# Optimization experiments

Measured on AMD Instinct MI355X. Metric: run time of the kernel, lower is better.

## Reference

```python
import jax, jax.numpy as jnp
import numpy as np

H = W = 64
C = 256
NUM_HEADS = 8

# Static index maps from AbsolutePositionalWeighting.__init__
_center_h = (H - 1) // 2
_center_w = (W - 1) // 2
_gi, _gj = np.meshgrid(np.arange(H), np.arange(W), indexing='ij')
_dx = _gi - _center_h
_dy = _gj - _center_w
DH = max(int(np.abs(_dx).max()), _center_h)
DW = max(int(np.abs(_dy).max()), _center_w)
DX_IDX = jnp.asarray(_dx + DH)  # (H, W)
DY_IDX = jnp.asarray(_dy + DW)  # (H, W)


def setup_inputs() -> dict:
    key = jax.random.key(0)
    ks = jax.random.split(key, 6)
    B, N = 16, H * W
    x1 = jax.random.normal(ks[0], (B, N, C), dtype=jnp.float32)
    x2 = jax.random.normal(ks[1], (B, N, C), dtype=jnp.float32)
    x3 = jax.random.normal(ks[2], (B, N, C), dtype=jnp.float32)
    pos_weights = 0.1 * jax.random.normal(ks[3], (2 * DH + 1, 2 * DW + 1, C), dtype=jnp.float32)
    lepe_w = 0.1 * jax.random.normal(ks[4], (C, 1, 3, 3), dtype=jnp.float32)  # depthwise OIHW
    lepe_b = 0.01 * jax.random.normal(ks[5], (C,), dtype=jnp.float32)
    return {"x1": x1, "x2": x2, "x3": x3, "pos_weights": pos_weights,
            "lepe_w": lepe_w, "lepe_b": lepe_b}


def reference(x1, x2, x3, pos_weights, lepe_w, lepe_b):
    b, n, c = x1.shape
    nh, hd = NUM_HEADS, c // NUM_HEADS

    q = jax.nn.elu(x1) + 1.0
    k = jax.nn.elu(x2) + 1.0
    v = x3

    # Positional gating: sigmoid(pos_weights gathered at per-pixel offsets) -> (N, C)
    pw = jax.nn.sigmoid(pos_weights[DX_IDX, DY_IDX, :]).reshape(n, c)
    q_rope = q * pw[None]  # (b, n, c)
    k_rope = k * pw[None]

    # Split heads: (b, n, nh, hd)
    q4 = q.reshape(b, n, nh, hd)
    k4 = k.reshape(b, n, nh, hd)
    v4 = v.reshape(b, n, nh, hd)
    qr4 = q_rope.reshape(b, n, nh, hd)
    kr4 = k_rope.reshape(b, n, nh, hd)

    # Normalizer z = 1 / (q . mean_n(k) + eps)
    k_mean = k4.mean(axis=1)  # (b, nh, hd)
    z = 1.0 / (jnp.einsum('bnhd,bhd->bnh', q4, k_mean) + 1e-6)

    # Linear attention: kv = (k_rope/sqrt(n))^T (v/sqrt(n)); out = q_rope @ kv * z
    kv = jnp.einsum('bnhd,bnhe->bhde', kr4, v4) / n  # (b, nh, hd, hd)
    attn = jnp.einsum('bnhd,bhde->bnhe', qr4, kv) * z[..., None]
    attn = attn.reshape(b, n, c)

    # LePE: depthwise 3x3 conv on v image (NCHW)
    v_img = v.reshape(b, H, W, c).transpose(0, 3, 1, 2)
    lepe = jax.lax.conv_general_dilated(
        v_img, lepe_w, window_strides=(1, 1), padding='SAME',
        feature_group_count=c,
        dimension_numbers=('NCHW', 'OIHW', 'NCHW'))
    lepe = lepe + lepe_b[None, :, None, None]
    lepe = lepe.transpose(0, 2, 3, 1).reshape(b, n, c)

    return attn + lepe
```

## Files before the change

kernel.cpp:

```cpp
#include <hip/hip_runtime.h>

#define BB 16
#define HIMG 64
#define WIMG 64
#define CC 256
#define NHEAD 8
#define HD 32
#define NN 4096
#define PWD 65
#define PADC 264
#define NCH 32

typedef short bf16x8 __attribute__((ext_vector_type(8)));
typedef float f32x4 __attribute__((ext_vector_type(4)));

__device__ __forceinline__ float elu1(float x) {
    return x > 0.0f ? x + 1.0f : __expf(x);
}
__device__ __forceinline__ float sigm(float x) {
    return 1.0f / (1.0f + __expf(-x));
}
__device__ __forceinline__ unsigned short f2bf(float f) {
    union { float f; unsigned int u; } v; v.f = f;
    unsigned int r = v.u + 0x7FFFu + ((v.u >> 16) & 1u);
    return (unsigned short)(r >> 16);
}
__device__ __forceinline__ float bf2f(unsigned short u) {
    union { unsigned int u; float f; } v; v.u = ((unsigned int)u) << 16;
    return v.f;
}

__global__ __launch_bounds__(256) void k0_pw(
    const float* __restrict__ posw, float* __restrict__ pw)
{
    const int gid = blockIdx.x * 256 + threadIdx.x;
    const int n = gid >> 6;
    const int p = gid & 63;
    const int ii = n >> 6, jj = n & 63;
    const float4 v = *(const float4*)(posw + (size_t)((ii + 1) * PWD + (jj + 1)) * CC + p * 4);
    float4 r;
    r.x = sigm(v.x); r.y = sigm(v.y); r.z = sigm(v.z); r.w = sigm(v.w);
    *(float4*)(pw + (size_t)n * CC + p * 4) = r;
}

__global__ __launch_bounds__(256) void k1_partial(
    const float* __restrict__ x2, const float* __restrict__ x3,
    const float* __restrict__ pw, float* __restrict__ pkv,
    float* __restrict__ pksum)
{
    const int t     = threadIdx.x;
    const int wv    = t >> 6;
    const int blk   = blockIdx.x;
    const int b     = blk >> 5;
    const int chunk = blk & 31;
    const int l     = t & 63;
    const int lr    = l & 15;
    const int lg    = l >> 4;

    const size_t bb = (size_t)b * NN * CC;

    f32x4 acc[2][4];
#pragma unroll
    for (int hh = 0; hh < 2; ++hh)
#pragma unroll
        for (int tl = 0; tl < 4; ++tl)
            acc[hh][tl] = (f32x4){0.f, 0.f, 0.f, 0.f};
    float ks[2][2] = {{0.f, 0.f}, {0.f, 0.f}};

    for (int s = 0; s < 4; ++s) {
        const int n0 = chunk * 128 + s * 32 + lg * 8;

        float kf[2][2][8], pf[2][2][8], vf[2][2][8];
#pragma unroll
        for (int hh = 0; hh < 2; ++hh)
#pragma unroll
            for (int dh = 0; dh < 2; ++dh) {
                const int ch = (wv * 2 + hh) * HD + dh * 16 + lr;
                const float* pk = x2 + bb + (size_t)n0 * CC + ch;
#pragma unroll
                for (int j = 0; j < 8; ++j) kf[hh][dh][j] = pk[j * CC];
            }
#pragma unroll
        for (int hh = 0; hh < 2; ++hh)
#pragma unroll
            for (int dh = 0; dh < 2; ++dh) {
                const int ch = (wv * 2 + hh) * HD + dh * 16 + lr;
                const float* pp = pw + (size_t)n0 * CC + ch;
#pragma unroll
                for (int j = 0; j < 8; ++j) pf[hh][dh][j] = pp[j * CC];
            }
#pragma unroll
        for (int hh = 0; hh < 2; ++hh)
#pragma unroll
            for (int eh = 0; eh < 2; ++eh) {
                const int ch = (wv * 2 + hh) * HD + eh * 16 + lr;
                const float* pv = x3 + bb + (size_t)n0 * CC + ch;
#pragma unroll
                for (int j = 0; j < 8; ++j) vf[hh][eh][j] = pv[j * CC];
            }

#pragma unroll
        for (int hh = 0; hh < 2; ++hh) {
            union { bf16x8 v8; unsigned short u[8]; } ka[2], vb[2];
#pragma unroll
            for (int dh = 0; dh < 2; ++dh)
#pragma unroll
                for (int j = 0; j < 8; ++j) {
                    const float e = elu1(kf[hh][dh][j]);
                    ks[hh][dh] += e;
                    ka[dh].u[j] = f2bf(e * pf[hh][dh][j]);
                }
#pragma unroll
            for (int eh = 0; eh < 2; ++eh)
#pragma unroll
                for (int j = 0; j < 8; ++j)
                    vb[eh].u[j] = f2bf(vf[hh][eh][j]);
#pragma unroll
            for (int dh = 0; dh < 2; ++dh)
#pragma unroll
                for (int eh = 0; eh < 2; ++eh)
                    acc[hh][dh * 2 + eh] = __builtin_amdgcn_mfma_f32_16x16x32_bf16(
                        ka[dh].v8, vb[eh].v8, acc[hh][dh * 2 + eh], 0, 0, 0);
        }
    }

#pragma unroll
    for (int hh = 0; hh < 2; ++hh) {
        float* dst = pkv + (size_t)blk * (NHEAD * HD * HD) + (wv * 2 + hh) * (HD * HD);
#pragma unroll
        for (int tl = 0; tl < 4; ++tl)
            *(f32x4*)(dst + tl * 256 + l * 4) = acc[hh][tl];
    }

#pragma unroll
    for (int hh = 0; hh < 2; ++hh)
#pragma unroll
        for (int dh = 0; dh < 2; ++dh) {
            ks[hh][dh] += __shfl_xor(ks[hh][dh], 16);
            ks[hh][dh] += __shfl_xor(ks[hh][dh], 32);
        }
    if (l < 16) {
#pragma unroll
        for (int hh = 0; hh < 2; ++hh)
#pragma unroll
            for (int dh = 0; dh < 2; ++dh)
                pksum[(size_t)blk * CC + (wv * 2 + hh) * HD + dh * 16 + l] = ks[hh][dh];
    }
}

__global__ __launch_bounds__(256) void k2_reduce(
    const float* __restrict__ pkv, const float* __restrict__ pksum,
    unsigned short* __restrict__ kvbT, float* __restrict__ kmean)
{
    const int gid = blockIdx.x * 256 + threadIdx.x;
    const int b = gid >> 13;
    const int o = gid & 8191;
    float s = 0.f;
#pragma unroll 4
    for (int c = 0; c < NCH; ++c)
        s += pkv[(size_t)(b * NCH + c) * (NHEAD * HD * HD) + o];
    const int hh   = o >> 10;
    const int r1   = o & 1023;
    const int tile = r1 >> 8;
    const int li   = (r1 >> 2) & 63;
    const int rg   = o & 3;
    const int d    = (tile >> 1) * 16 + (li >> 4) * 4 + rg;
    const int e    = (tile & 1) * 16 + (li & 15);
    kvbT[(((size_t)b * NHEAD + hh) * HD + e) * HD + d] = f2bf(s * (1.0f / NN));
    if (o < CC) {
        float ss = 0.f;
#pragma unroll 4
        for (int c = 0; c < NCH; ++c)
            ss += pksum[(size_t)(b * NCH + c) * CC + o];
        kmean[b * CC + o] = ss * (1.0f / NN);
    }
}

__global__ __launch_bounds__(256) void k3_out(
    const float* __restrict__ x1, const float* __restrict__ x3,
    const float* __restrict__ pw, const unsigned short* __restrict__ kvbT,
    const float* __restrict__ kmean, const float* __restrict__ lw,
    const float* __restrict__ lb, float* __restrict__ out)
{
    const int blk  = blockIdx.x;
    const int b    = blk >> 8;
    const int irow = (blk >> 2) & 63;
    const int jq   = blk & 3;
    const int j0   = jq << 4;
    const int t    = threadIdx.x;

    __shared__ unsigned short qr_bf[16 * PADC];
    __shared__ unsigned short attn_bf[16 * PADC];

    float wreg[9];
#pragma unroll
    for (int q = 0; q < 9; ++q) wreg[q] = lw[t * 9 + q];
    const float bias = lb[t];

    {
        const int p    = t & 63;
        const int pixo = t >> 6;
        const float4 km4 = *(const float4*)(kmean + b * CC + p * 4);
        const float* x1b = x1 + ((size_t)b * NN + (size_t)irow * 64 + j0) * CC;
        const float* pwb = pw + ((size_t)irow * 64 + j0) * CC;
        float4 xv[4], pvv[4];
#pragma unroll
        for (int s = 0; s < 4; ++s)
            xv[s] = *(const float4*)(x1b + (size_t)(s * 4 + pixo) * CC + p * 4);
#pragma unroll
        for (int s = 0; s < 4; ++s)
            pvv[s] = *(const float4*)(pwb + (size_t)(s * 4 + pixo) * CC + p * 4);
#pragma unroll
        for (int s = 0; s < 4; ++s) {
            const int pix = s * 4 + pixo;
            float4 q4;
            q4.x = elu1(xv[s].x); q4.y = elu1(xv[s].y);
            q4.z = elu1(xv[s].z); q4.w = elu1(xv[s].w);
            float zp = q4.x * km4.x + q4.y * km4.y + q4.z * km4.z + q4.w * km4.w;
            zp += __shfl_xor(zp, 1);
            zp += __shfl_xor(zp, 2);
            zp += __shfl_xor(zp, 4);
            const float zin = 1.0f / (zp + 1e-6f);
            ushort4 u;
            u.x = f2bf(q4.x * pvv[s].x * zin);
            u.y = f2bf(q4.y * pvv[s].y * zin);
            u.z = f2bf(q4.z * pvv[s].z * zin);
            u.w = f2bf(q4.w * pvv[s].w * zin);
            *(ushort4*)(&qr_bf[pix * PADC + p * 4]) = u;
        }
    }

    const bool hasU = irow > 0, hasD = irow < 63;
    const float* rU = x3 + ((size_t)b * NN + (size_t)(irow - 1) * 64 + j0) * CC + t;
    const float* rM = x3 + ((size_t)b * NN + (size_t)irow * 64 + j0) * CC + t;
    const float* rD = x3 + ((size_t)b * NN + (size_t)(irow + 1) * 64 + j0) * CC + t;

    float cu[2][10], cm[2][10], cd[2][10];
#pragma unroll
    for (int tt = 0; tt < 2; ++tt)
#pragma unroll
        for (int q = 0; q < 10; ++q) {
            const int col = tt * 8 + q - 1;
            const int g   = j0 + col;
            const bool ok = (g >= 0) && (g < 64);
            const long off = (long)col * CC;
            cm[tt][q] = ok ? rM[off] : 0.f;
            cu[tt][q] = (ok && hasU) ? rU[off] : 0.f;
            cd[tt][q] = (ok && hasD) ? rD[off] : 0.f;
        }

    __syncthreads();

    {
        const int w  = t >> 6;
        const int l  = t & 63;
        const int lr = l & 15;
        const int lg = l >> 4;

        bf16x8 af0 = *(const bf16x8*)(&qr_bf[lr * PADC + (w * 2 + 0) * HD + lg * 8]);
        bf16x8 af1 = *(const bf16x8*)(&qr_bf[lr * PADC + (w * 2 + 1) * HD + lg * 8]);

        f32x4 acc[4];
#pragma unroll
        for (int ct = 0; ct < 4; ++ct) {
            const int head = w * 2 + (ct >> 1);
            const int cl   = (ct & 1) * 16 + lr;
            const bf16x8 bf = *(const bf16x8*)(kvbT +
                (((size_t)b * NHEAD + head) * HD + cl) * HD + lg * 8);
            f32x4 z4 = {0.f, 0.f, 0.f, 0.f};
            acc[ct] = __builtin_amdgcn_mfma_f32_16x16x32_bf16(
                (ct < 2) ? af0 : af1, bf, z4, 0, 0, 0);
        }
#pragma unroll
        for (int ct = 0; ct < 4; ++ct) {
            const int c = (w * 2 + (ct >> 1)) * HD + (ct & 1) * 16 + lr;
#pragma unroll
            for (int r = 0; r < 4; ++r)
                attn_bf[(lg * 4 + r) * PADC + c] = f2bf(acc[ct][r]);
        }
    }

    __syncthreads();

    float* ob = out + ((size_t)b * NN + (size_t)irow * 64 + j0) * CC + t;
#pragma unroll
    for (int tt = 0; tt < 2; ++tt) {
#pragma unroll
        for (int q = 0; q < 8; ++q) {
            const int jl = tt * 8 + q;
            float lepe = bias
                + wreg[0] * cu[tt][q] + wreg[1] * cu[tt][q + 1] + wreg[2] * cu[tt][q + 2]
                + wreg[3] * cm[tt][q] + wreg[4] * cm[tt][q + 1] + wreg[5] * cm[tt][q + 2]
                + wreg[6] * cd[tt][q] + wreg[7] * cd[tt][q + 1] + wreg[8] * cd[tt][q + 2];
            __builtin_nontemporal_store(bf2f(attn_bf[jl * PADC + t]) + lepe,
                                        ob + (long)jl * CC);
        }
    }
}

extern "C" void kernel_launch(void* const* d_in, const int* in_sizes, int n_in,
                              void* d_out, int out_size, void* d_ws, size_t ws_size,
                              hipStream_t stream) {
    const float* x1   = (const float*)d_in[0];
    const float* x2   = (const float*)d_in[1];
    const float* x3   = (const float*)d_in[2];
    const float* posw = (const float*)d_in[3];
    const float* lw   = (const float*)d_in[4];
    const float* lb   = (const float*)d_in[5];
    float* out = (float*)d_out;

    const size_t pw_sz = (size_t)NN * CC;
    float* pwb   = (float*)d_ws;
    float* pkv   = pwb + pw_sz;
    float* pksum = pkv + (size_t)16 * NCH * 8192;
    float* kmean = pksum + (size_t)16 * NCH * 256;
    unsigned short* kvbT = (unsigned short*)(kmean + (size_t)16 * 256);

    k0_pw<<<1024, 256, 0, stream>>>(posw, pwb);
    k1_partial<<<BB * NCH, 256, 0, stream>>>(x2, x3, pwb, pkv, pksum);
    k2_reduce<<<512, 256, 0, stream>>>(pkv, pksum, kvbT, kmean);
    k3_out<<<BB * 256, 256, 0, stream>>>(x1, x3, pwb, kvbT, kmean, lw, lb, out);
}
```

Measured before the change: 82.20 us.

## Split fused output kernel into attention and LePE kernels via bf16 workspace

The fused output kernel is split in two. The first kernel computes the gated q times kv MFMA product and writes the attention result as bf16 to a workspace buffer. The second kernel reads that buffer and adds the depthwise 3x3 conv and bias. The split is meant to lower per-kernel register and LDS pressure and so raise occupancy. In exchange it adds a 32 MB bf16 write plus readback and one extra launch, and it falls back to the fused kernel when the workspace is too small.

```diff
diff --git a/kernel.cpp b/kernel.cpp
--- a/kernel.cpp
+++ b/kernel.cpp
@@ -176,11 +176,10 @@
     }
 }
 
-__global__ __launch_bounds__(256) void k3_out(
-    const float* __restrict__ x1, const float* __restrict__ x3,
-    const float* __restrict__ pw, const unsigned short* __restrict__ kvbT,
-    const float* __restrict__ kmean, const float* __restrict__ lw,
-    const float* __restrict__ lb, float* __restrict__ out)
+__global__ __launch_bounds__(256) void k3a_attn(
+    const float* __restrict__ x1, const float* __restrict__ pw,
+    const unsigned short* __restrict__ kvbT, const float* __restrict__ kmean,
+    unsigned short* __restrict__ attn_ws)
 {
     const int blk  = blockIdx.x;
     const int b    = blk >> 8;
@@ -191,11 +190,6 @@
 
     __shared__ unsigned short qr_bf[16 * PADC];
     __shared__ unsigned short attn_bf[16 * PADC];
-
-    float wreg[9];
-#pragma unroll
-    for (int q = 0; q < 9; ++q) wreg[q] = lw[t * 9 + q];
-    const float bias = lb[t];
 
     {
         const int p    = t & 63;
@@ -229,6 +223,153 @@
             *(ushort4*)(&qr_bf[pix * PADC + p * 4]) = u;
         }
     }
+    __syncthreads();
+
+    {
+        const int w  = t >> 6;
+        const int l  = t & 63;
+        const int lr = l & 15;
+        const int lg = l >> 4;
+
+        bf16x8 af0 = *(const bf16x8*)(&qr_bf[lr * PADC + (w * 2 + 0) * HD + lg * 8]);
+        bf16x8 af1 = *(const bf16x8*)(&qr_bf[lr * PADC + (w * 2 + 1) * HD + lg * 8]);
+
+        f32x4 acc[4];
+#pragma unroll
+        for (int ct = 0; ct < 4; ++ct) {
+            const int head = w * 2 + (ct >> 1);
+            const int cl   = (ct & 1) * 16 + lr;
+            const bf16x8 bf = *(const bf16x8*)(kvbT +
+                (((size_t)b * NHEAD + head) * HD + cl) * HD + lg * 8);
+            f32x4 z4 = {0.f, 0.f, 0.f, 0.f};
+            acc[ct] = __builtin_amdgcn_mfma_f32_16x16x32_bf16(
+                (ct < 2) ? af0 : af1, bf, z4, 0, 0, 0);
+        }
+#pragma unroll
+        for (int ct = 0; ct < 4; ++ct) {
+            const int c = (w * 2 + (ct >> 1)) * HD + (ct & 1) * 16 + lr;
+#pragma unroll
+            for (int r = 0; r < 4; ++r)
+                attn_bf[(lg * 4 + r) * PADC + c] = f2bf(acc[ct][r]);
+        }
+    }
+    __syncthreads();
+
+    unsigned short* ob = attn_ws + ((size_t)b * NN + (size_t)irow * 64 + j0) * CC + t;
+#pragma unroll
+    for (int jl = 0; jl < 16; ++jl)
+        ob[(size_t)jl * CC] = attn_bf[jl * PADC + t];
+}
+
+__global__ __launch_bounds__(256) void k3b_lepe(
+    const float* __restrict__ x3, const unsigned short* __restrict__ attn_ws,
+    const float* __restrict__ lw, const float* __restrict__ lb,
+    float* __restrict__ out)
+{
+    const int blk  = blockIdx.x;
+    const int b    = blk >> 8;
+    const int irow = (blk >> 2) & 63;
+    const int jq   = blk & 3;
+    const int j0   = jq << 4;
+    const int t    = threadIdx.x;
+
+    float wreg[9];
+#pragma unroll
+    for (int q = 0; q < 9; ++q) wreg[q] = lw[t * 9 + q];
+    const float bias = lb[t];
+
+    const bool hasU = irow > 0, hasD = irow < 63;
+    const float* rU = x3 + ((size_t)b * NN + (size_t)(irow - 1) * 64 + j0) * CC + t;
+    const float* rM = x3 + ((size_t)b * NN + (size_t)irow * 64 + j0) * CC + t;
+    const float* rD = x3 + ((size_t)b * NN + (size_t)(irow + 1) * 64 + j0) * CC + t;
+    const unsigned short* pa = attn_ws + ((size_t)b * NN + (size_t)irow * 64 + j0) * CC + t;
+
+    unsigned short av[16];
+#pragma unroll
+    for (int jl = 0; jl < 16; ++jl) av[jl] = pa[(size_t)jl * CC];
+
+    float cu[2][10], cm[2][10], cd[2][10];
+#pragma unroll
+    for (int tt = 0; tt < 2; ++tt)
+#pragma unroll
+        for (int q = 0; q < 10; ++q) {
+            const int col = tt * 8 + q - 1;
+            const int g   = j0 + col;
+            const bool ok = (g >= 0) && (g < 64);
+            const long off = (long)col * CC;
+            cm[tt][q] = ok ? rM[off] : 0.f;
+            cu[tt][q] = (ok && hasU) ? rU[off] : 0.f;
+            cd[tt][q] = (ok && hasD) ? rD[off] : 0.f;
+        }
+
+    float* ob = out + ((size_t)b * NN + (size_t)irow * 64 + j0) * CC + t;
+#pragma unroll
+    for (int tt = 0; tt < 2; ++tt) {
+#pragma unroll
+        for (int q = 0; q < 8; ++q) {
+            const int jl = tt * 8 + q;
+            float lepe = bias
+                + wreg[0] * cu[tt][q] + wreg[1] * cu[tt][q + 1] + wreg[2] * cu[tt][q + 2]
+                + wreg[3] * cm[tt][q] + wreg[4] * cm[tt][q + 1] + wreg[5] * cm[tt][q + 2]
+                + wreg[6] * cd[tt][q] + wreg[7] * cd[tt][q + 1] + wreg[8] * cd[tt][q + 2];
+            __builtin_nontemporal_store(bf2f(av[jl]) + lepe, ob + (long)jl * CC);
+        }
+    }
+}
+
+__global__ __launch_bounds__(256) void k3_out(
+    const float* __restrict__ x1, const float* __restrict__ x3,
+    const float* __restrict__ pw, const unsigned short* __restrict__ kvbT,
+    const float* __restrict__ kmean, const float* __restrict__ lw,
+    const float* __restrict__ lb, float* __restrict__ out)
+{
+    const int blk  = blockIdx.x;
+    const int b    = blk >> 8;
+    const int irow = (blk >> 2) & 63;
+    const int jq   = blk & 3;
+    const int j0   = jq << 4;
+    const int t    = threadIdx.x;
+
+    __shared__ unsigned short qr_bf[16 * PADC];
+    __shared__ unsigned short attn_bf[16 * PADC];
+
+    float wreg[9];
+#pragma unroll
+    for (int q = 0; q < 9; ++q) wreg[q] = lw[t * 9 + q];
+    const float bias = lb[t];
+
+    {
+        const int p    = t & 63;
+        const int pixo = t >> 6;
+        const float4 km4 = *(const float4*)(kmean + b * CC + p * 4);
+        const float* x1b = x1 + ((size_t)b * NN + (size_t)irow * 64 + j0) * CC;
+        const float* pwb = pw + ((size_t)irow * 64 + j0) * CC;
+        float4 xv[4], pvv[4];
+#pragma unroll
+        for (int s = 0; s < 4; ++s)
+            xv[s] = *(const float4*)(x1b + (size_t)(s * 4 + pixo) * CC + p * 4);
+#pragma unroll
+        for (int s = 0; s < 4; ++s)
+            pvv[s] = *(const float4*)(pwb + (size_t)(s * 4 + pixo) * CC + p * 4);
+#pragma unroll
+        for (int s = 0; s < 4; ++s) {
+            const int pix = s * 4 + pixo;
+            float4 q4;
+            q4.x = elu1(xv[s].x); q4.y = elu1(xv[s].y);
+            q4.z = elu1(xv[s].z); q4.w = elu1(xv[s].w);
+            float zp = q4.x * km4.x + q4.y * km4.y + q4.z * km4.z + q4.w * km4.w;
+            zp += __shfl_xor(zp, 1);
+            zp += __shfl_xor(zp, 2);
+            zp += __shfl_xor(zp, 4);
+            const float zin = 1.0f / (zp + 1e-6f);
+            ushort4 u;
+            u.x = f2bf(q4.x * pvv[s].x * zin);
+            u.y = f2bf(q4.y * pvv[s].y * zin);
+            u.z = f2bf(q4.z * pvv[s].z * zin);
+            u.w = f2bf(q4.w * pvv[s].w * zin);
+            *(ushort4*)(&qr_bf[pix * PADC + p * 4]) = u;
+        }
+    }
 
     const bool hasU = irow > 0, hasD = irow < 63;
     const float* rU = x3 + ((size_t)b * NN + (size_t)(irow - 1) * 64 + j0) * CC + t;
@@ -309,15 +450,30 @@
     const float* lb   = (const float*)d_in[5];
     float* out = (float*)d_out;
 
-    const size_t pw_sz = (size_t)NN * CC;
+    const size_t pw_f  = (size_t)NN * CC;
+    const size_t pkv_f = (size_t)16 * NCH * 8192;
+    const size_t pks_f = (size_t)16 * NCH * 256;
+    const size_t km_f  = (size_t)16 * 256;
+    const size_t kvbT_u = (size_t)16 * 8192;
+    const size_t attn_u = (size_t)16 * NN * CC;
+
     float* pwb   = (float*)d_ws;
-    float* pkv   = pwb + pw_sz;
-    float* pksum = pkv + (size_t)16 * NCH * 8192;
-    float* kmean = pksum + (size_t)16 * NCH * 256;
-    unsigned short* kvbT = (unsigned short*)(kmean + (size_t)16 * 256);
+    float* pkv   = pwb + pw_f;
+    float* pksum = pkv + pkv_f;
+    float* kmean = pksum + pks_f;
+    unsigned short* kvbT = (unsigned short*)(kmean + km_f);
+    unsigned short* attn_ws = kvbT + kvbT_u;
+
+    const size_t need_split = (pw_f + pkv_f + pks_f + km_f) * sizeof(float) +
+                              (kvbT_u + attn_u) * sizeof(unsigned short);
 
     k0_pw<<<1024, 256, 0, stream>>>(posw, pwb);
     k1_partial<<<BB * NCH, 256, 0, stream>>>(x2, x3, pwb, pkv, pksum);
     k2_reduce<<<512, 256, 0, stream>>>(pkv, pksum, kvbT, kmean);
-    k3_out<<<BB * 256, 256, 0, stream>>>(x1, x3, pwb, kvbT, kmean, lw, lb, out);
-}
+    if (ws_size >= need_split) {
+        k3a_attn<<<BB * 256, 256, 0, stream>>>(x1, pwb, kvbT, kmean, attn_ws);
+        k3b_lepe<<<BB * 256, 256, 0, stream>>>(x3, attn_ws, lw, lb, out);
+    } else {
+        k3_out<<<BB * 256, 256, 0, stream>>>(x1, x3, pwb, kvbT, kmean, lw, lb, out);
+    }
+}
```

Measured after the change: 94.40 us. 14.8% more time.
